# Performance work log

Hardware: AMD Instinct MI355X
Metric: run time of the kernel (lower is better)

Reference implementation:

```python
import jax, jax.numpy as jnp
import numpy as np

D_K = 64

def setup_inputs() -> dict:
    key = jax.random.key(0)
    ks = jax.random.split(key, 9)
    B, S, D = 8, 2048, 512
    d_k, d_v = 64, 64
    return {
        "q_in": jax.random.normal(ks[0], (B, S, D), jnp.float32),
        "k_in": jax.random.normal(ks[1], (B, S, D), jnp.float32),
        "v_in": jax.random.normal(ks[2], (B, S, D), jnp.float32),
        "Wq": jax.random.normal(ks[3], (D, d_k), jnp.float32) * 0.05,
        "bq": jax.random.normal(ks[4], (d_k,), jnp.float32) * 0.05,
        "Wk": jax.random.normal(ks[5], (D, d_k), jnp.float32) * 0.05,
        "bk": jax.random.normal(ks[6], (d_k,), jnp.float32) * 0.05,
        "Wv": jax.random.normal(ks[7], (D, d_v), jnp.float32) * 0.05,
        "bv": jax.random.normal(ks[8], (d_v,), jnp.float32) * 0.05,
    }

def reference(q_in, k_in, v_in, Wq, bq, Wk, bk, Wv, bv):
    # Dense projections: x @ W + b
    q = jnp.einsum('bsd,dk->bsk', q_in, Wq) + bq  # [B,S,d_k]
    k = jnp.einsum('bsd,dk->bsk', k_in, Wk) + bk  # [B,S,d_k]
    v = jnp.einsum('bsd,dv->bsv', v_in, Wv) + bv  # [B,S,d_v]
    scale = 1.0 / np.sqrt(D_K).astype(np.float32)
    scores = jnp.einsum('bqk,bsk->bqs', q, k) * scale  # [B,S,S]
    attn = jax.nn.softmax(scores, axis=-1)
    return jnp.einsum('bqs,bsv->bqv', attn, v)  # [B,S,d_v]
```

## Files before the change

### kernel.cpp

```cpp
#include <hip/hip_runtime.h>
#include <hip/hip_bf16.h>
#include <cstdint>

typedef __attribute__((ext_vector_type(8))) short short8;
typedef __attribute__((ext_vector_type(16))) float f32x16;

#if __has_builtin(__builtin_amdgcn_exp2f)
#define EXP2F(x) __builtin_amdgcn_exp2f(x)
#else
#define EXP2F(x) exp2f(x)
#endif

#define MFMA32(A, B, C) __builtin_amdgcn_mfma_f32_32x32x16_bf16((A), (B), (C), 0, 0, 0)

__device__ __forceinline__ unsigned short f2bf(float f) {
  unsigned int u = __builtin_bit_cast(unsigned int, f);
  u += 0x7FFFu + ((u >> 16) & 1u);
  return (unsigned short)(u >> 16);
}

__global__ __launch_bounds__(256) void prep_wt(
    const float* __restrict__ Wq, const float* __restrict__ Wk,
    const float* __restrict__ Wv, unsigned short* __restrict__ Wt)
{
  int idx = blockIdx.x * 256 + threadIdx.x;
  int which = idx >> 15;
  int rem = idx & 32767;
  int n = rem >> 9;
  int k = rem & 511;
  const float* W = (which == 0) ? Wq : (which == 1) ? Wk : Wv;
  Wt[idx] = f2bf(W[k * 64 + n]);
}

__global__ __launch_bounds__(256, 3) void proj_kernel(
    const float* __restrict__ qin, const float* __restrict__ kin,
    const float* __restrict__ vin, const unsigned short* __restrict__ Wt,
    const float* __restrict__ bq, const float* __restrict__ bk,
    const float* __restrict__ bv,
    unsigned short* __restrict__ Qo, unsigned short* __restrict__ Ko,
    unsigned short* __restrict__ Vto)
{
  __shared__ char smem_raw[16384];
  float* red = (float*)smem_raw;
  unsigned short* TB = (unsigned short*)smem_raw;

  const int which = blockIdx.y;
  const float* X    = (which == 0) ? qin : (which == 1) ? kin : vin;
  const float* bias = (which == 0) ? bq  : (which == 1) ? bk  : bv;

  const int lane = threadIdx.x & 63;
  const int wv = threadIdx.x >> 6;
  const int h = lane >> 5, l31 = lane & 31;
  const int grp = wv & 1;
  const int kh = wv >> 1;
  const int rowbase = blockIdx.x * 64 + grp * 32;

  const float* xrow = X + (size_t)(rowbase + l31) * 512 + kh * 256 + h * 8;
  const unsigned short* wbase = Wt + (size_t)which * 64 * 512 + kh * 256 + h * 8;
  const unsigned short* w0 = wbase + (size_t)l31 * 512;
  const unsigned short* w1 = w0 + 32 * 512;

  f32x16 acc0 = {}, acc1 = {};
  #pragma unroll 4
  for (int kc = 0; kc < 16; ++kc) {
    float4 a0 = *(const float4*)(xrow + kc * 16);
    float4 a1 = *(const float4*)(xrow + kc * 16 + 4);
    short8 af = { (short)f2bf(a0.x), (short)f2bf(a0.y), (short)f2bf(a0.z), (short)f2bf(a0.w),
                  (short)f2bf(a1.x), (short)f2bf(a1.y), (short)f2bf(a1.z), (short)f2bf(a1.w) };
    short8 b0 = *(const short8*)(w0 + kc * 16);
    short8 b1 = *(const short8*)(w1 + kc * 16);
    acc0 = MFMA32(af, b0, acc0);
    acc1 = MFMA32(af, b1, acc1);
  }

  if (kh == 1) {
    #pragma unroll
    for (int r = 0; r < 16; ++r) {
      int row = (r & 3) + 8 * (r >> 2) + 4 * h;
      red[grp * 2048 + row * 64 + l31]      = acc0[r];
      red[grp * 2048 + row * 64 + l31 + 32] = acc1[r];
    }
  }
  __syncthreads();
  if (kh == 0) {
    #pragma unroll
    for (int r = 0; r < 16; ++r) {
      int row = (r & 3) + 8 * (r >> 2) + 4 * h;
      acc0[r] += red[grp * 2048 + row * 64 + l31];
      acc1[r] += red[grp * 2048 + row * 64 + l31 + 32];
    }
  }

  const float bias0 = bias[l31], bias1 = bias[l31 + 32];

  if (which < 2) {
    if (kh == 0) {
      const float scale = which ? 1.0f : 0.18033688f;
      unsigned short* Y = which ? Ko : Qo;
      #pragma unroll
      for (int r = 0; r < 16; ++r) {
        int row = (r & 3) + 8 * (r >> 2) + 4 * h;
        size_t base = (size_t)(rowbase + row) * 64;
        Y[base + l31]      = f2bf((acc0[r] + bias0) * scale);
        Y[base + l31 + 32] = f2bf((acc1[r] + bias1) * scale);
      }
    }
  } else {
    __syncthreads();
    if (kh == 0) {
      #pragma unroll
      for (int r = 0; r < 16; ++r) {
        int row = (r & 3) + 8 * (r >> 2) + 4 * h;
        int sl = grp * 32 + row;
        TB[l31 * 68 + sl]        = f2bf(acc0[r] + bias0);
        TB[(l31 + 32) * 68 + sl] = f2bf(acc1[r] + bias1);
      }
    }
    __syncthreads();
    int bidx = blockIdx.x >> 5;
    int s0 = (blockIdx.x & 31) * 64;
    for (int i = threadIdx.x; i < 64 * 16; i += 256) {
      int n = i >> 4, c = i & 15;
      ushort4 v4 = *(const ushort4*)(TB + n * 68 + c * 4);
      *(ushort4*)(Vto + ((size_t)bidx * 64 + n) * 2048 + s0 + c * 4) = v4;
    }
  }
}

__global__ __launch_bounds__(512, 2) void attn_kernel(
    const unsigned short* __restrict__ Q, const unsigned short* __restrict__ K,
    const unsigned short* __restrict__ Vt, float* __restrict__ out)
{
  __shared__ float ObS[4][16][64];
  __shared__ float MpS[4][64];
  __shared__ float LpS[4][64];

  const int tid = threadIdx.x;
  const int lane = tid & 63, w = tid >> 6;
  const int h = lane >> 5, l31 = lane & 31;
  const int b = blockIdx.y;
  const int q0 = blockIdx.x * 64;

  short8 qf[2][4];
  #pragma unroll
  for (int qt = 0; qt < 2; ++qt) {
    const unsigned short* qp = Q + ((size_t)(b * 2048 + q0 + qt * 32 + l31)) * 64 + h * 8;
    #pragma unroll
    for (int c = 0; c < 4; ++c) qf[qt][c] = *(const short8*)(qp + c * 16);
  }

  f32x16 o00 = {}, o01 = {}, o10 = {}, o11 = {};
  float m0 = -1e30f, m1 = -1e30f, ls0 = 0.f, ls1 = 0.f;

  for (int st = 0; st < 8; ++st) {
    const int kb = w * 256 + st * 32;
    short8 kf[4];
    const unsigned short* kp = K + ((size_t)(b * 2048 + kb + l31)) * 64 + h * 8;
    #pragma unroll
    for (int c = 0; c < 4; ++c) kf[c] = *(const short8*)(kp + c * 16);
    short8 vf0[2], vf1[2];
    {
      const unsigned short* vp0 = Vt + ((size_t)(b * 64 + l31)) * 2048 + kb + h * 8;
      const unsigned short* vp1 = Vt + ((size_t)(b * 64 + 32 + l31)) * 2048 + kb + h * 8;
      vf0[0] = *(const short8*)(vp0);  vf0[1] = *(const short8*)(vp0 + 16);
      vf1[0] = *(const short8*)(vp1);  vf1[1] = *(const short8*)(vp1 + 16);
    }
    #pragma unroll
    for (int qt = 0; qt < 2; ++qt) {
      f32x16 sT = {};
      #pragma unroll
      for (int c = 0; c < 4; ++c) sT = MFMA32(kf[c], qf[qt][c], sT);
      float mx = sT[0];
      #pragma unroll
      for (int r = 1; r < 16; ++r) mx = fmaxf(mx, sT[r]);
      mx = fmaxf(mx, __shfl_xor(mx, 32, 64));
      float mold = qt ? m1 : m0;
      float mnew = fmaxf(mold, mx);
      float alpha = EXP2F(mold - mnew);
      float rs = 0.f;
      float p[16];
      #pragma unroll
      for (int r = 0; r < 16; ++r) { p[r] = EXP2F(sT[r] - mnew); rs += p[r]; }
      rs += __shfl_xor(rs, 32, 64);
      unsigned int pk[8];
      #pragma unroll
      for (int i = 0; i < 8; ++i)
        pk[i] = (unsigned int)f2bf(p[2 * i]) | ((unsigned int)f2bf(p[2 * i + 1]) << 16);
      unsigned int ex[8];
      #pragma unroll
      for (int i = 0; i < 8; ++i) ex[i] = (unsigned int)__shfl_xor((int)pk[i], 32, 64);
      uint4 cc0, cc1;
      if (h == 0) { cc0 = make_uint4(pk[0], pk[1], ex[0], ex[1]); cc1 = make_uint4(pk[4], pk[5], ex[4], ex[5]); }
      else        { cc0 = make_uint4(ex[2], ex[3], pk[2], pk[3]); cc1 = make_uint4(ex[6], ex[7], pk[6], pk[7]); }
      short8 P0 = __builtin_bit_cast(short8, cc0);
      short8 P1 = __builtin_bit_cast(short8, cc1);
      if (qt == 0) {
        m0 = mnew; ls0 = ls0 * alpha + rs;
        o00 *= alpha; o10 *= alpha;
        o00 = MFMA32(vf0[0], P0, o00); o00 = MFMA32(vf0[1], P1, o00);
        o10 = MFMA32(vf1[0], P0, o10); o10 = MFMA32(vf1[1], P1, o10);
      } else {
        m1 = mnew; ls1 = ls1 * alpha + rs;
        o01 *= alpha; o11 *= alpha;
        o01 = MFMA32(vf0[0], P0, o01); o01 = MFMA32(vf0[1], P1, o01);
        o11 = MFMA32(vf1[0], P0, o11); o11 = MFMA32(vf1[1], P1, o11);
      }
    }
  }

  for (int half = 4; half > 0; half >>= 1) {
    const bool writer = (w >= half) && (w < 2 * half);
    const bool merger = (w < half);
    __syncthreads();
    if (writer && h == 0) {
      MpS[w - half][l31] = m0;      LpS[w - half][l31] = ls0;
      MpS[w - half][32 + l31] = m1; LpS[w - half][32 + l31] = ls1;
    }
    __syncthreads();
    float fb0 = 0.f, fb1 = 0.f;
    if (merger) {
      float pm0 = MpS[w][l31],      pl0 = LpS[w][l31];
      float pm1 = MpS[w][32 + l31], pl1 = LpS[w][32 + l31];
      float nm0 = fmaxf(m0, pm0), nm1 = fmaxf(m1, pm1);
      float fa0 = EXP2F(m0 - nm0); fb0 = EXP2F(pm0 - nm0);
      float fa1 = EXP2F(m1 - nm1); fb1 = EXP2F(pm1 - nm1);
      m0 = nm0; m1 = nm1;
      ls0 = ls0 * fa0 + pl0 * fb0; ls1 = ls1 * fa1 + pl1 * fb1;
      o00 *= fa0; o10 *= fa0; o01 *= fa1; o11 *= fa1;
    }
    __syncthreads();
    if (writer) {
      #pragma unroll
      for (int r = 0; r < 16; ++r) ObS[w - half][r][lane] = o00[r]; }
    __syncthreads();
    if (merger) {
      #pragma unroll
      for (int r = 0; r < 16; ++r) o00[r] += ObS[w][r][lane] * fb0; }
    __syncthreads();
    if (writer) {
      #pragma unroll
      for (int r = 0; r < 16; ++r) ObS[w - half][r][lane] = o01[r]; }
    __syncthreads();
    if (merger) {
      #pragma unroll
      for (int r = 0; r < 16; ++r) o01[r] += ObS[w][r][lane] * fb1; }
    __syncthreads();
    if (writer) {
      #pragma unroll
      for (int r = 0; r < 16; ++r) ObS[w - half][r][lane] = o10[r]; }
    __syncthreads();
    if (merger) {
      #pragma unroll
      for (int r = 0; r < 16; ++r) o10[r] += ObS[w][r][lane] * fb0; }
    __syncthreads();
    if (writer) {
      #pragma unroll
      for (int r = 0; r < 16; ++r) ObS[w - half][r][lane] = o11[r]; }
    __syncthreads();
    if (merger) {
      #pragma unroll
      for (int r = 0; r < 16; ++r) o11[r] += ObS[w][r][lane] * fb1; }
  }

  if (w == 0) {
    float i0 = 1.0f / ls0, i1 = 1.0f / ls1;
    o00 *= i0; o10 *= i0; o01 *= i1; o11 *= i1;
    #pragma unroll
    for (int qt = 0; qt < 2; ++qt) {
      int q = qt * 32 + l31;
      float* ob = out + ((size_t)(b * 2048 + q0 + q)) * 64 + 4 * h;
      const f32x16 a = qt ? o01 : o00;
      const f32x16 c = qt ? o11 : o10;
      #pragma unroll
      for (int g = 0; g < 4; ++g) {
        *(float4*)(ob + 8 * g)      = make_float4(a[4*g], a[4*g+1], a[4*g+2], a[4*g+3]);
        *(float4*)(ob + 32 + 8 * g) = make_float4(c[4*g], c[4*g+1], c[4*g+2], c[4*g+3]);
      }
    }
  }
}

extern "C" void kernel_launch(void* const* d_in, const int* in_sizes, int n_in,
                              void* d_out, int out_size, void* d_ws, size_t ws_size,
                              hipStream_t stream) {
  const float* qin = (const float*)d_in[0];
  const float* kin = (const float*)d_in[1];
  const float* vin = (const float*)d_in[2];
  const float* Wq  = (const float*)d_in[3];
  const float* bq  = (const float*)d_in[4];
  const float* Wk  = (const float*)d_in[5];
  const float* bk  = (const float*)d_in[6];
  const float* Wv  = (const float*)d_in[7];
  const float* bv  = (const float*)d_in[8];

  unsigned short* Qo  = (unsigned short*)d_ws;
  unsigned short* Ko  = Qo + (size_t)16384 * 64;
  unsigned short* Vto = Ko + (size_t)16384 * 64;
  unsigned short* Wt  = Vto + (size_t)8 * 64 * 2048;
  float* out = (float*)d_out;

  hipLaunchKernelGGL(prep_wt, dim3(384), dim3(256), 0, stream, Wq, Wk, Wv, Wt);
  hipLaunchKernelGGL(proj_kernel, dim3(256, 3), dim3(256), 0, stream,
                     qin, kin, vin, Wt, bq, bk, bv, Qo, Ko, Vto);
  hipLaunchKernelGGL(attn_kernel, dim3(32, 8), dim3(512), 0, stream, Qo, Ko, Vto, out);
}
```

Before: 171.5 us.

## Stage X tiles through LDS in projection kernel and split waves over N

The projection kernel now loads each 64x128 chunk of X cooperatively with row-coalesced float4 loads, converts it to bf16 into shared memory, and has the four waves read A fragments from LDS. Work is split by output column half instead of by K half, so the cross-wave reduction through shared memory goes away. This targets poorly coalesced strided global reads of X and the reduction overhead. In exchange it adds per-chunk barriers and LDS traffic, and each wave now issues a serial chain of MFMAs on a single accumulator.

```diff
diff --git a/kernel.cpp b/kernel.cpp
--- a/kernel.cpp
+++ b/kernel.cpp
@@ -40,89 +40,73 @@
     unsigned short* __restrict__ Qo, unsigned short* __restrict__ Ko,
     unsigned short* __restrict__ Vto)
 {
-  __shared__ char smem_raw[16384];
-  float* red = (float*)smem_raw;
-  unsigned short* TB = (unsigned short*)smem_raw;
+  __shared__ unsigned short Xs[64 * 136];
 
   const int which = blockIdx.y;
   const float* X    = (which == 0) ? qin : (which == 1) ? kin : vin;
   const float* bias = (which == 0) ? bq  : (which == 1) ? bk  : bv;
 
-  const int lane = threadIdx.x & 63;
-  const int wv = threadIdx.x >> 6;
+  const int tid = threadIdx.x;
+  const int lane = tid & 63, wv = tid >> 6;
   const int h = lane >> 5, l31 = lane & 31;
-  const int grp = wv & 1;
-  const int kh = wv >> 1;
-  const int rowbase = blockIdx.x * 64 + grp * 32;
-
-  const float* xrow = X + (size_t)(rowbase + l31) * 512 + kh * 256 + h * 8;
-  const unsigned short* wbase = Wt + (size_t)which * 64 * 512 + kh * 256 + h * 8;
-  const unsigned short* w0 = wbase + (size_t)l31 * 512;
-  const unsigned short* w1 = w0 + 32 * 512;
-
-  f32x16 acc0 = {}, acc1 = {};
-  #pragma unroll 4
-  for (int kc = 0; kc < 16; ++kc) {
-    float4 a0 = *(const float4*)(xrow + kc * 16);
-    float4 a1 = *(const float4*)(xrow + kc * 16 + 4);
-    short8 af = { (short)f2bf(a0.x), (short)f2bf(a0.y), (short)f2bf(a0.z), (short)f2bf(a0.w),
-                  (short)f2bf(a1.x), (short)f2bf(a1.y), (short)f2bf(a1.z), (short)f2bf(a1.w) };
-    short8 b0 = *(const short8*)(w0 + kc * 16);
-    short8 b1 = *(const short8*)(w1 + kc * 16);
-    acc0 = MFMA32(af, b0, acc0);
-    acc1 = MFMA32(af, b1, acc1);
-  }
-
-  if (kh == 1) {
+  const int grp = wv & 1, nh = wv >> 1;
+  const int m0 = blockIdx.x * 64;
+
+  const unsigned short* wcol =
+      Wt + (size_t)which * 64 * 512 + (size_t)(nh * 32 + l31) * 512 + h * 8;
+
+  const int srow = tid >> 5;
+  const int skoff = tid & 31;
+  const float* xg = X + (size_t)(m0 + srow) * 512 + skoff * 4;
+
+  f32x16 acc = {};
+  for (int c = 0; c < 4; ++c) {
+    __syncthreads();
+    #pragma unroll
+    for (int j = 0; j < 8; ++j) {
+      float4 a = *(const float4*)(xg + (size_t)(8 * j) * 512 + c * 128);
+      unsigned int w0 = (unsigned int)f2bf(a.x) | ((unsigned int)f2bf(a.y) << 16);
+      unsigned int w1 = (unsigned int)f2bf(a.z) | ((unsigned int)f2bf(a.w) << 16);
+      uint2 pw; pw.x = w0; pw.y = w1;
+      *(uint2*)(&Xs[(srow + 8 * j) * 136 + skoff * 4]) = pw;
+    }
+    __syncthreads();
+    const unsigned short* arow = &Xs[(grp * 32 + l31) * 136 + h * 8];
+    const unsigned short* wk = wcol + c * 128;
+    #pragma unroll
+    for (int ks = 0; ks < 8; ++ks) {
+      short8 af = *(const short8*)(arow + ks * 16);
+      short8 bf = *(const short8*)(wk + ks * 16);
+      acc = MFMA32(af, bf, acc);
+    }
+  }
+
+  const float bv0 = bias[nh * 32 + l31];
+
+  if (which < 2) {
+    const float scale = which ? 1.0f : 0.18033688f;
+    unsigned short* Y = which ? Ko : Qo;
     #pragma unroll
     for (int r = 0; r < 16; ++r) {
       int row = (r & 3) + 8 * (r >> 2) + 4 * h;
-      red[grp * 2048 + row * 64 + l31]      = acc0[r];
-      red[grp * 2048 + row * 64 + l31 + 32] = acc1[r];
-    }
-  }
-  __syncthreads();
-  if (kh == 0) {
+      Y[(size_t)(m0 + grp * 32 + row) * 64 + nh * 32 + l31] =
+          f2bf((acc[r] + bv0) * scale);
+    }
+  } else {
+    __syncthreads();
+    unsigned short* TB = Xs;
     #pragma unroll
     for (int r = 0; r < 16; ++r) {
       int row = (r & 3) + 8 * (r >> 2) + 4 * h;
-      acc0[r] += red[grp * 2048 + row * 64 + l31];
-      acc1[r] += red[grp * 2048 + row * 64 + l31 + 32];
-    }
-  }
-
-  const float bias0 = bias[l31], bias1 = bias[l31 + 32];
-
-  if (which < 2) {
-    if (kh == 0) {
-      const float scale = which ? 1.0f : 0.18033688f;
-      unsigned short* Y = which ? Ko : Qo;
-      #pragma unroll
-      for (int r = 0; r < 16; ++r) {
-        int row = (r & 3) + 8 * (r >> 2) + 4 * h;
-        size_t base = (size_t)(rowbase + row) * 64;
-        Y[base + l31]      = f2bf((acc0[r] + bias0) * scale);
-        Y[base + l31 + 32] = f2bf((acc1[r] + bias1) * scale);
-      }
-    }
-  } else {
-    __syncthreads();
-    if (kh == 0) {
-      #pragma unroll
-      for (int r = 0; r < 16; ++r) {
-        int row = (r & 3) + 8 * (r >> 2) + 4 * h;
-        int sl = grp * 32 + row;
-        TB[l31 * 68 + sl]        = f2bf(acc0[r] + bias0);
-        TB[(l31 + 32) * 68 + sl] = f2bf(acc1[r] + bias1);
-      }
+      TB[(nh * 32 + l31) * 68 + grp * 32 + row] = f2bf(acc[r] + bv0);
     }
     __syncthreads();
     int bidx = blockIdx.x >> 5;
     int s0 = (blockIdx.x & 31) * 64;
-    for (int i = threadIdx.x; i < 64 * 16; i += 256) {
-      int n = i >> 4, c = i & 15;
-      ushort4 v4 = *(const ushort4*)(TB + n * 68 + c * 4);
-      *(ushort4*)(Vto + ((size_t)bidx * 64 + n) * 2048 + s0 + c * 4) = v4;
+    for (int i = tid; i < 64 * 16; i += 256) {
+      int n = i >> 4, cs = i & 15;
+      ushort4 v4 = *(const ushort4*)(TB + n * 68 + cs * 4);
+      *(ushort4*)(Vto + ((size_t)bidx * 64 + n) * 2048 + s0 + cs * 4) = v4;
     }
   }
 }
```

After: 162.3 us. 5.4% less time.
